# Kernel optimization log

Measured on AMD Instinct MI355X. Metric: run time of the kernel, lower is better.

The kernel has to match this reference:

```python
import jax, jax.numpy as jnp
import numpy as np

VOCAB = 100000; EMB = 256; HID = 512; H2 = HID // 2; C = 12; T = 2048
START = 10; STOP = 11  # '<END>' and '<STOP>' share index 11
NEG = -10000.0


def setup_inputs() -> dict:
    key = jax.random.key(0)
    ks = jax.random.split(key, 16)
    s = 1.0 / np.sqrt(H2)
    u = lambda k, shape: jax.random.uniform(k, shape, jnp.float32, -s, s)
    inp = {
        "sentence": jax.random.randint(ks[0], (T,), 0, VOCAB),
        "emb": jax.random.normal(ks[1], (VOCAB, EMB), jnp.float32),
        "Wih_f": u(ks[2], (4 * H2, EMB)),
        "Whh_f": u(ks[3], (4 * H2, H2)),
        "bih_f": u(ks[4], (4 * H2,)),
        "bhh_f": u(ks[5], (4 * H2,)),
        "Wih_b": u(ks[6], (4 * H2, EMB)),
        "Whh_b": u(ks[7], (4 * H2, H2)),
        "bih_b": u(ks[8], (4 * H2,)),
        "bhh_b": u(ks[9], (4 * H2,)),
        "Wlin": u(ks[10], (C, HID)),
        "blin": u(ks[11], (C,)),
        "h0": jax.random.normal(ks[12], (2, H2), jnp.float32),  # init_hidden()
        "c0": jax.random.normal(ks[13], (2, H2), jnp.float32),
    }
    trans = jax.random.normal(ks[14], (C, C), jnp.float32)
    # transitions[START, :] = transitions[:, END] = -10000 (as in __init__)
    trans = trans.at[START, :].set(NEG).at[:, STOP].set(NEG)
    inp["transitions"] = trans
    return inp


def _lstm_dir(x, Wih, Whh, bih, bhh, h, c, reverse):
    # PyTorch LSTM gate order: i, f, g, o
    def step(carry, xt):
        h, c = carry
        g = xt @ Wih.T + bih + h @ Whh.T + bhh  # [4*H2]
        i, f, gg, o = jnp.split(g, 4)
        c = jax.nn.sigmoid(f) * c + jax.nn.sigmoid(i) * jnp.tanh(gg)
        h = jax.nn.sigmoid(o) * jnp.tanh(c)
        return (h, c), h
    _, hs = jax.lax.scan(step, (h, c), x, reverse=reverse)
    return hs  # [T, H2]


def reference(sentence, emb, Wih_f, Whh_f, bih_f, bhh_f,
              Wih_b, Whh_b, bih_b, bhh_b, Wlin, blin, h0, c0, transitions):
    # _get_lstm_features
    x = emb[sentence]  # [T, EMB]
    hf = _lstm_dir(x, Wih_f, Whh_f, bih_f, bhh_f, h0[0], c0[0], False)
    hb = _lstm_dir(x, Wih_b, Whh_b, bih_b, bhh_b, h0[1], c0[1], True)
    feats = jnp.concatenate([hf, hb], axis=-1) @ Wlin.T + blin  # [T, C]

    # _viterbi: vectorized over tags, scanned over time
    fv0 = jnp.full((C,), NEG, jnp.float32).at[START].set(0.0)

    def vstep(fv, feat):
        scores = fv[None, :] + transitions  # [next, prev]
        bp = jnp.argmax(scores, axis=1)     # best prev tag for each next tag
        return jnp.max(scores, axis=1) + feat, bp

    fv, bps = jax.lax.scan(vstep, fv0, feats)  # bps: [T, C]
    terminal = fv + transitions[STOP]
    best = jnp.argmax(terminal)
    path_score = terminal[best]

    # backtrace: path[t] = tag at time t
    def back(tag, bp):
        return bp[tag], tag
    _, path = jax.lax.scan(back, best, bps, reverse=True)
    return path_score, path
```

## Files before the change

### kernel.cpp

```cpp
#include <hip/hip_runtime.h>
#include <hip/hip_fp16.h>

#define TT   2048
#define EMBD 256
#define HD   256
#define NG   1024
#define NC   12
#define NEGV -10000.0f

typedef _Float16 half2v __attribute__((ext_vector_type(2)));
typedef _Float16 f16x8  __attribute__((ext_vector_type(8)));
typedef float    f32x4  __attribute__((ext_vector_type(4)));

__device__ float g_P[2 * TT * NG];
__device__ float g_HS[2 * TT * HD];
__device__ float g_FE[TT * NC];

__device__ __forceinline__ unsigned int f2h2(float a, float b) {
  half2v h; h.x = (_Float16)a; h.y = (_Float16)b;
  return __builtin_bit_cast(unsigned int, h);
}
__device__ __forceinline__ f16x8 asf16x8(uint4 v) { return __builtin_bit_cast(f16x8, v); }
__device__ __forceinline__ float fsigmoid(float x) { return 1.0f / (1.0f + __expf(-x)); }
__device__ __forceinline__ float ftanh(float x) {
  float a = fabsf(x);
  float e = __expf(-2.0f * a);
  float r = (1.0f - e) / (1.0f + e);
  return copysignf(r, x);
}


__global__ __launch_bounds__(256) void k_input(
    const int* __restrict__ sent, const float* __restrict__ emb,
    const float* __restrict__ WihF, const float* __restrict__ bihF,
    const float* __restrict__ bhhF,
    const float* __restrict__ WihB, const float* __restrict__ bihB,
    const float* __restrict__ bhhB)
{
  const int d  = blockIdx.x & 1;
  const int t0 = (blockIdx.x >> 1) * 16;
  const float* Wih = d ? WihB : WihF;
  const float* bih = d ? bihB : bihF;
  const float* bhh = d ? bhhB : bhhF;
  __shared__ float xs[16][EMBD];
  for (int i = threadIdx.x; i < 16 * (EMBD / 4); i += 256) {
    const int tt = i >> 6, e4 = i & 63;
    reinterpret_cast<float4*>(xs[tt])[e4] =
        reinterpret_cast<const float4*>(emb + (size_t)sent[t0 + tt] * EMBD)[e4];
  }
  __syncthreads();
  for (int gg = 0; gg < 4; ++gg) {
    const int g = threadIdx.x + gg * 256;
    const float bias = bih[g] + bhh[g];
    float acc[16];
#pragma unroll
    for (int tt = 0; tt < 16; ++tt) acc[tt] = 0.0f;
    const float* wr = Wih + (size_t)g * EMBD;
    for (int e = 0; e < EMBD; e += 4) {
      const float4 w = *reinterpret_cast<const float4*>(wr + e);
#pragma unroll
      for (int tt = 0; tt < 16; ++tt) {
        acc[tt] += w.x * xs[tt][e] + w.y * xs[tt][e + 1]
                 + w.z * xs[tt][e + 2] + w.w * xs[tt][e + 3];
      }
    }
    const int u = g & 255, ga = g >> 8;
    const int rp = 4 * u + ga;
    float* Pg = g_P + ((size_t)d * TT + t0) * NG + rp;
#pragma unroll
    for (int tt = 0; tt < 16; ++tt) Pg[(size_t)tt * NG] = acc[tt] + bias;
  }
}

__global__ __launch_bounds__(512, 2) void k_rec(
    const float* __restrict__ WhhF, const float* __restrict__ WhhB,
    const float* __restrict__ h0g, const float* __restrict__ c0g)
{
  __shared__ __align__(16) uint4 wlds[8][8][2][64];
  __shared__ __align__(16) unsigned short h2[2][HD];
  __shared__ __align__(16) float gates[256][4];

  const int d = blockIdx.x;
  const float* __restrict__ Whh = d ? WhhB : WhhF;
  const int tid  = threadIdx.x;
  const int w    = tid >> 6;
  const int lane = tid & 63;
  const int kg   = lane >> 4;
  const int m    = lane & 15;
  const int lg   = m >> 2, ga = m & 3;

  uint4 Ares[8][6];
#pragma unroll
  for (int rt = 0; rt < 8; ++rt) {
    const int orow = (ga << 8) + (w << 5) + (rt << 2) + lg;
    const float* wr = Whh + (size_t)orow * HD;
#pragma unroll
    for (int kt = 0; kt < 8; ++kt) {
      const int k0 = (kt << 5) + (kg << 3);
      const float4 x0 = *reinterpret_cast<const float4*>(wr + k0);
      const float4 x1 = *reinterpret_cast<const float4*>(wr + k0 + 4);
      uint4 f;
      f.x = f2h2(x0.x, x0.y); f.y = f2h2(x0.z, x0.w);
      f.z = f2h2(x1.x, x1.y); f.w = f2h2(x1.z, x1.w);
      if (kt < 6) Ares[rt][kt] = f;
      else        wlds[w][rt][kt - 6][lane] = f;
    }
  }
  if (tid < HD / 2)
    reinterpret_cast<unsigned int*>(h2[0])[tid] =
        f2h2(h0g[d * HD + 2 * tid], h0g[d * HD + 2 * tid + 1]);
  float c = (tid < 256) ? c0g[d * HD + tid] : 0.0f;
  __syncthreads();

  const float* Pbase = g_P + (size_t)d * TT * NG + 4 * tid;
  int t = d ? (TT - 1) : 0;
  const int tstep = d ? -1 : 1;
  float4 Pc = {0.f, 0.f, 0.f, 0.f};
  if (tid < 256) Pc = *reinterpret_cast<const float4*>(Pbase + (size_t)t * NG);
  int p = 0;

  for (int it = 0; it < TT; ++it, t += tstep) {
    f16x8 bf[8];
#pragma unroll
    for (int kt = 0; kt < 8; ++kt)
      bf[kt] = asf16x8(*reinterpret_cast<const uint4*>(&h2[p][(kt << 5) + (kg << 3)]));

#pragma unroll
    for (int rt = 0; rt < 8; ++rt) {
      const uint4 sa = wlds[w][rt][0][lane];
      const uint4 sb = wlds[w][rt][1][lane];
      f32x4 acc = {0.f, 0.f, 0.f, 0.f};
#pragma unroll
      for (int kt = 0; kt < 6; ++kt)
        acc = __builtin_amdgcn_mfma_f32_16x16x32_f16(asf16x8(Ares[rt][kt]), bf[kt], acc, 0, 0, 0);
      acc = __builtin_amdgcn_mfma_f32_16x16x32_f16(asf16x8(sa), bf[6], acc, 0, 0, 0);
      acc = __builtin_amdgcn_mfma_f32_16x16x32_f16(asf16x8(sb), bf[7], acc, 0, 0, 0);
      if (m == 0)
        *reinterpret_cast<float4*>(gates[(w << 5) + (rt << 2) + kg]) =
            __builtin_bit_cast(float4, acc);
    }
    asm volatile("s_waitcnt lgkmcnt(0)" ::: "memory");
    __builtin_amdgcn_s_barrier();
    __builtin_amdgcn_sched_barrier(0);

    if (tid < 256) {
      const float4 gv = *reinterpret_cast<const float4*>(gates[tid]);
      const float gi = gv.x + Pc.x;
      const float gf = gv.y + Pc.y;
      const float gz = gv.z + Pc.z;
      const float go = gv.w + Pc.w;
      c = fsigmoid(gf) * c + fsigmoid(gi) * ftanh(gz);
      const float hh = fsigmoid(go) * ftanh(c);
      g_HS[((size_t)d * TT + t) * HD + tid] = hh;
      h2[p ^ 1][tid] = __builtin_bit_cast(unsigned short, (_Float16)hh);
      const int tn = (it + 1 < TT) ? (t + tstep) : t;
      Pc = *reinterpret_cast<const float4*>(Pbase + (size_t)tn * NG);
    }
    p ^= 1;
    asm volatile("s_waitcnt lgkmcnt(0)" ::: "memory");
    __builtin_amdgcn_s_barrier();
    __builtin_amdgcn_sched_barrier(0);
  }
}

__global__ __launch_bounds__(256) void k_feats(
    const float* __restrict__ Wlin, const float* __restrict__ blin)
{
  const int gid = blockIdx.x * 256 + threadIdx.x;
  if (gid >= TT * NC) return;
  const int t = gid / NC, cc = gid - t * NC;
  const float* hf = g_HS + (size_t)t * HD;
  const float* hb = g_HS + ((size_t)TT + t) * HD;
  const float* wr = Wlin + cc * 512;
  float acc = blin[cc];
  for (int j = 0; j < HD; j += 4) {
    const float4 w = *reinterpret_cast<const float4*>(wr + j);
    acc += w.x * hf[j] + w.y * hf[j + 1] + w.z * hf[j + 2] + w.w * hf[j + 3];
  }
  for (int j = 0; j < HD; j += 4) {
    const float4 w = *reinterpret_cast<const float4*>(wr + 256 + j);
    acc += w.x * hb[j] + w.y * hb[j + 1] + w.z * hb[j + 2] + w.w * hb[j + 3];
  }
  g_FE[gid] = acc;
}

__global__ __launch_bounds__(64) void k_vit(
    const float* __restrict__ trans, float* __restrict__ out)
{
  const int lane = threadIdx.x;
  const bool act = lane < NC;
  __shared__ unsigned char bp[TT][NC];
  float Trow[NC];
#pragma unroll
  for (int i = 0; i < NC; ++i) Trow[i] = act ? trans[lane * NC + i] : NEGV;
  float fv[NC];
#pragma unroll
  for (int i = 0; i < NC; ++i) fv[i] = (i == 10) ? 0.0f : NEGV;

  float f0 = act ? g_FE[lane] : 0.0f;
  float f1 = act ? g_FE[NC + lane] : 0.0f;
  for (int t = 0; t < TT; ++t) {
    const float feat = f0;
    f0 = f1;
    f1 = (act && t + 2 < TT) ? g_FE[(t + 2) * NC + lane] : 0.0f;
    float best = fv[0] + Trow[0]; int bi = 0;
#pragma unroll
    for (int i = 1; i < NC; ++i) {
      const float s = fv[i] + Trow[i];
      if (s > best) { best = s; bi = i; }
    }
    if (act) bp[t][lane] = (unsigned char)bi;
    const float nf = best + feat;
#pragma unroll
    for (int i = 0; i < NC; ++i) fv[i] = __shfl(nf, i);
  }
  const float term = act ? (fv[lane] + trans[11 * NC + lane]) : -3.0e38f;
  float tv[NC];
#pragma unroll
  for (int i = 0; i < NC; ++i) tv[i] = __shfl(term, i);
  if (lane == 0) {
    float bs = tv[0]; int bt = 0;
#pragma unroll
    for (int i = 1; i < NC; ++i) if (tv[i] > bs) { bs = tv[i]; bt = i; }
    out[0] = bs;
    int tag = bt;
    for (int t = TT - 1; t >= 0; --t) {
      out[1 + t] = (float)tag;
      tag = bp[t][tag];
    }
  }
}

extern "C" void kernel_launch(void* const* d_in, const int* in_sizes, int n_in,
                              void* d_out, int out_size, void* d_ws, size_t ws_size,
                              hipStream_t stream) {
  const int*   sent = (const int*)d_in[0];
  const float* emb  = (const float*)d_in[1];
  const float* WihF = (const float*)d_in[2];
  const float* WhhF = (const float*)d_in[3];
  const float* bihF = (const float*)d_in[4];
  const float* bhhF = (const float*)d_in[5];
  const float* WihB = (const float*)d_in[6];
  const float* WhhB = (const float*)d_in[7];
  const float* bihB = (const float*)d_in[8];
  const float* bhhB = (const float*)d_in[9];
  const float* Wlin = (const float*)d_in[10];
  const float* blin = (const float*)d_in[11];
  const float* h0g  = (const float*)d_in[12];
  const float* c0g  = (const float*)d_in[13];
  const float* trans= (const float*)d_in[14];
  (void)d_ws; (void)ws_size; (void)in_sizes; (void)n_in; (void)out_size;

  k_input<<<dim3(2 * (TT / 16)), dim3(256), 0, stream>>>(
      sent, emb, WihF, bihF, bhhF, WihB, bihB, bhhB);

  k_rec<<<dim3(2), dim3(512), 0, stream>>>(WhhF, WhhB, h0g, c0g);

  k_feats<<<dim3((TT * NC + 255) / 256), dim3(256), 0, stream>>>(Wlin, blin);

  k_vit<<<dim3(1), dim3(64), 0, stream>>>(trans, (float*)d_out);
}
```

Measured before the change: 4.358 ms.

## Spill part of recurrent weights to global memory and software-pipeline weight loads

The recurrent LSTM kernel now keeps the kt=6 weight tiles in LDS and moves most kt=7 tiles to a global buffer, prefetching both two row-tiles ahead through a rotating register ring so the loads overlap the MFMA chain. This reduces the LDS footprint per block and hides load latency, at the cost of global or L2 reads inside the serial time loop. The Viterbi kernel also keeps one forward-variable value per lane and broadcasts it with shuffles inside the max loop, instead of rebuilding a full per-lane array after each step.

```diff
diff --git a/kernel.cpp b/kernel.cpp
--- a/kernel.cpp
+++ b/kernel.cpp
@@ -15,6 +15,7 @@
 __device__ float g_P[2 * TT * NG];
 __device__ float g_HS[2 * TT * HD];
 __device__ float g_FE[TT * NC];
+__device__ uint4 g_W7[2 * 8 * 6 * 64];
 
 __device__ __forceinline__ unsigned int f2h2(float a, float b) {
   half2v h; h.x = (_Float16)a; h.y = (_Float16)b;
@@ -76,8 +77,8 @@
     const float* __restrict__ WhhF, const float* __restrict__ WhhB,
     const float* __restrict__ h0g, const float* __restrict__ c0g)
 {
-  __shared__ __align__(16) uint4 wlds[8][8][2][64];
-  __shared__ __align__(16) unsigned short h2[2][HD];
+  __shared__ __align__(16) uint4 wlds[8][10][64];
+  __shared__ __align__(16) unsigned short h2[2][256];
   __shared__ __align__(16) float gates[256][4];
 
   const int d = blockIdx.x;
@@ -102,17 +103,22 @@
       uint4 f;
       f.x = f2h2(x0.x, x0.y); f.y = f2h2(x0.z, x0.w);
       f.z = f2h2(x1.x, x1.y); f.w = f2h2(x1.z, x1.w);
-      if (kt < 6) Ares[rt][kt] = f;
-      else        wlds[w][rt][kt - 6][lane] = f;
-    }
-  }
-  if (tid < HD / 2)
+      if (kt < 6)            Ares[rt][kt] = f;
+      else if (kt == 6)      wlds[w][rt][lane] = f;
+      else if (rt < 2)       wlds[w][8 + rt][lane] = f;
+      else                   g_W7[(size_t)(((d << 3) + w) * 6 + (rt - 2)) * 64 + lane] = f;
+    }
+  }
+  if (tid < 128)
     reinterpret_cast<unsigned int*>(h2[0])[tid] =
         f2h2(h0g[d * HD + 2 * tid], h0g[d * HD + 2 * tid + 1]);
   float c = (tid < 256) ? c0g[d * HD + tid] : 0.0f;
   __syncthreads();
 
   const float* Pbase = g_P + (size_t)d * TT * NG + 4 * tid;
+  const uint4* wl = &wlds[w][0][lane];
+  const unsigned int w7base = (unsigned int)((((d << 3) + w) * 6) * 64 + lane);
+
   int t = d ? (TT - 1) : 0;
   const int tstep = d ? -1 : 1;
   float4 Pc = {0.f, 0.f, 0.f, 0.f};
@@ -120,21 +126,30 @@
   int p = 0;
 
   for (int it = 0; it < TT; ++it, t += tstep) {
+    unsigned int w7o = w7base;
+    asm volatile("" : "+v"(w7o));
+
     f16x8 bf[8];
 #pragma unroll
     for (int kt = 0; kt < 8; ++kt)
       bf[kt] = asf16x8(*reinterpret_cast<const uint4*>(&h2[p][(kt << 5) + (kg << 3)]));
 
+    uint4 s6r[3], s7r[3];
+    s6r[0] = wl[0 * 64];  s6r[1] = wl[1 * 64];
+    s7r[0] = wl[8 * 64];  s7r[1] = wl[9 * 64];
+
 #pragma unroll
     for (int rt = 0; rt < 8; ++rt) {
-      const uint4 sa = wlds[w][rt][0][lane];
-      const uint4 sb = wlds[w][rt][1][lane];
+      if (rt + 2 < 8) {
+        s6r[(rt + 2) % 3] = wl[(rt + 2) * 64];
+        s7r[(rt + 2) % 3] = g_W7[w7o + rt * 64];
+      }
       f32x4 acc = {0.f, 0.f, 0.f, 0.f};
 #pragma unroll
       for (int kt = 0; kt < 6; ++kt)
         acc = __builtin_amdgcn_mfma_f32_16x16x32_f16(asf16x8(Ares[rt][kt]), bf[kt], acc, 0, 0, 0);
-      acc = __builtin_amdgcn_mfma_f32_16x16x32_f16(asf16x8(sa), bf[6], acc, 0, 0, 0);
-      acc = __builtin_amdgcn_mfma_f32_16x16x32_f16(asf16x8(sb), bf[7], acc, 0, 0, 0);
+      acc = __builtin_amdgcn_mfma_f32_16x16x32_f16(asf16x8(s6r[rt % 3]), bf[6], acc, 0, 0, 0);
+      acc = __builtin_amdgcn_mfma_f32_16x16x32_f16(asf16x8(s7r[rt % 3]), bf[7], acc, 0, 0, 0);
       if (m == 0)
         *reinterpret_cast<float4*>(gates[(w << 5) + (rt << 2) + kg]) =
             __builtin_bit_cast(float4, acc);
@@ -193,9 +208,7 @@
   float Trow[NC];
 #pragma unroll
   for (int i = 0; i < NC; ++i) Trow[i] = act ? trans[lane * NC + i] : NEGV;
-  float fv[NC];
-#pragma unroll
-  for (int i = 0; i < NC; ++i) fv[i] = (i == 10) ? 0.0f : NEGV;
+  float fv = (lane == 10) ? 0.0f : NEGV;
 
   float f0 = act ? g_FE[lane] : 0.0f;
   float f1 = act ? g_FE[NC + lane] : 0.0f;
@@ -203,18 +216,16 @@
     const float feat = f0;
     f0 = f1;
     f1 = (act && t + 2 < TT) ? g_FE[(t + 2) * NC + lane] : 0.0f;
-    float best = fv[0] + Trow[0]; int bi = 0;
+    float best = __shfl(fv, 0) + Trow[0]; int bi = 0;
 #pragma unroll
     for (int i = 1; i < NC; ++i) {
-      const float s = fv[i] + Trow[i];
+      const float s = __shfl(fv, i) + Trow[i];
       if (s > best) { best = s; bi = i; }
     }
     if (act) bp[t][lane] = (unsigned char)bi;
-    const float nf = best + feat;
-#pragma unroll
-    for (int i = 0; i < NC; ++i) fv[i] = __shfl(nf, i);
-  }
-  const float term = act ? (fv[lane] + trans[11 * NC + lane]) : -3.0e38f;
+    fv = best + feat;
+  }
+  const float term = act ? (fv + trans[11 * NC + lane]) : -3.0e38f;
   float tv[NC];
 #pragma unroll
   for (int i = 0; i < NC; ++i) tv[i] = __shfl(term, i);
```

Measured after the change: 5.657 ms. 1.3x slower.
